# Optimization experiments

Measured on AMD Instinct MI355X. Metric: run time of the kernel, lower is better.

The kernel has to match this reference:

```python
import jax, jax.numpy as jnp
import numpy as np

NUM_HEADS = 8
HIDDEN_DIM = 64
N_REAL = 30000
N_VIRT = 2000
N_NODES = N_REAL + N_VIRT
N_EDGES = 512000
VOCAB = 100000


def setup_inputs() -> dict:
    key = jax.random.key(0)
    k1, k2, k3, k4, k5 = jax.random.split(key, 5)
    features = jax.random.normal(k1, (VOCAB, HIDDEN_DIM), dtype=jnp.float32)
    virtue_emb = jax.random.normal(k2, (N_VIRT, HIDDEN_DIM), dtype=jnp.float32)  # nn.Embedding weight ~ N(0,1)
    cnodes = jax.random.randint(k3, (N_REAL,), 0, VOCAB, dtype=jnp.int64)
    src = jax.random.randint(k4, (N_EDGES,), 0, N_NODES, dtype=jnp.int64)
    dst = jax.random.randint(k5, (N_EDGES,), 0, N_NODES, dtype=jnp.int64)
    vm_idx = jnp.arange(N_VIRT, dtype=jnp.int64) + N_REAL  # virtual nodes are appended after real nodes
    return {"features": features, "virtue_emb": virtue_emb, "cnodes": cnodes,
            "src": src, "dst": dst, "vm_idx": vm_idx}


def _edge_softmax(e, dst, n_nodes):
    # DGL edge_softmax: softmax over incoming edges of each destination node.
    m = jax.ops.segment_max(e, dst, num_segments=n_nodes)          # [N,H,1]
    ex = jnp.exp(e - m[dst])                                       # [E,H,1]
    s = jax.ops.segment_sum(ex, dst, num_segments=n_nodes)        # [N,H,1]
    return ex / s[dst]


def reference(features, virtue_emb, cnodes, src, dst, vm_idx):
    real_ndata = features[cnodes]                                  # [R,D] F.embedding
    ndata = jnp.concatenate([real_ndata, virtue_emb], axis=0)      # [N,D]
    n = ndata.shape[0]
    # agg_type='neighbor': cat([h]*H, dim=1).view(-1,H,D) == broadcast along head dim
    nft = jnp.broadcast_to(ndata[:, None, :], (n, NUM_HEADS, HIDDEN_DIM))
    e = jnp.ones((src.shape[0], NUM_HEADS, 1), dtype=ndata.dtype)
    eft = _edge_softmax(e, dst, n)                                 # [E,H,1]
    new_nft = jax.ops.segment_sum(nft[src] * eft, dst, num_segments=n)      # round 1: u_mul_e / sum
    final_nft = jax.ops.segment_sum(new_nft[src] * eft, dst, num_segments=n)  # round 2
    return final_nft[vm_idx]                                       # [V,H,D]
```

## Files before the change

### kernel.cpp

```cpp
#include <hip/hip_runtime.h>

constexpr int HEADS  = 8;
constexpr int DIM    = 64;
constexpr int NREAL  = 30000;
constexpr int NVIRT  = 2000;
constexpr int NNODES = NREAL + NVIRT;
constexpr int NEDGES = 512000;
constexpr int STRIDE = 64;

typedef _Float16 half4 __attribute__((ext_vector_type(4)));


__global__ __launch_bounds__(256) void k_prep(const float* __restrict__ features,
                                              const float* __restrict__ virtue,
                                              const int* __restrict__ cnodes,
                                              const int* __restrict__ src,
                                              const int* __restrict__ dst,
                                              _Float16* __restrict__ ndata,
                                              int* __restrict__ cnt,
                                              unsigned char* __restrict__ mark,
                                              unsigned short* __restrict__ slots) {
  int i = blockIdx.x * blockDim.x + threadIdx.x;
  {
    int node = i >> 4;
    int q    = i & 15;
    const float4* srcp = (node < NREAL)
        ? (const float4*)(features + (long)cnodes[node] * DIM)
        : (const float4*)(virtue + (long)(node - NREAL) * DIM);
    float4 v = srcp[q];
    half4 h = { (_Float16)v.x, (_Float16)v.y, (_Float16)v.z, (_Float16)v.w };
    ((half4*)(ndata + (long)node * DIM))[q] = h;
  }
  {
    int d = dst[i];
    int s = src[i];
    int pos = atomicAdd(&cnt[d], 1);
    if (pos < STRIDE) slots[(long)d * STRIDE + pos] = (unsigned short)s;
    if (d >= NREAL) mark[s] = 1;
  }
}

__global__ __launch_bounds__(256) void k_agg1(const int* __restrict__ cnt,
                                              const unsigned char* __restrict__ mark,
                                              const unsigned short* __restrict__ slots,
                                              const _Float16* __restrict__ ndata,
                                              float* __restrict__ new_nft) {
  int node = blockIdx.x * 4 + (threadIdx.x >> 6);
  if (node >= NNODES) return;
  int lane = threadIdx.x & 63;
  int q = lane >> 4;
  int l = lane & 15;
  unsigned char m = mark[node];
  int deg = cnt[node];
  int myidx = (int)slots[(long)node * STRIDE + lane];
  if (!m) return;
  if (deg > STRIDE) deg = STRIDE;
  float4 acc  = make_float4(0.f, 0.f, 0.f, 0.f);
  float4 acc2 = make_float4(0.f, 0.f, 0.f, 0.f);
  const half4* nd = (const half4*)ndata;
#pragma unroll
  for (int u = 0; u < 8; ++u) {
    int ka = u * 8 + q;
    int kb = u * 8 + q + 4;
    int sa = __shfl(myidx, ka);
    int sb = __shfl(myidx, kb);
    if (ka < deg) {
      half4 v = nd[(long)sa * 16 + l];
      acc.x += (float)v.x; acc.y += (float)v.y; acc.z += (float)v.z; acc.w += (float)v.w;
    }
    if (kb < deg) {
      half4 v = nd[(long)sb * 16 + l];
      acc2.x += (float)v.x; acc2.y += (float)v.y; acc2.z += (float)v.z; acc2.w += (float)v.w;
    }
  }
  acc.x += acc2.x; acc.y += acc2.y; acc.z += acc2.z; acc.w += acc2.w;
  acc.x += __shfl_xor(acc.x, 16); acc.y += __shfl_xor(acc.y, 16);
  acc.z += __shfl_xor(acc.z, 16); acc.w += __shfl_xor(acc.w, 16);
  acc.x += __shfl_xor(acc.x, 32); acc.y += __shfl_xor(acc.y, 32);
  acc.z += __shfl_xor(acc.z, 32); acc.w += __shfl_xor(acc.w, 32);
  if (q == 0) {
    float inv = (deg > 0) ? 1.0f / (float)deg : 0.0f;
    acc.x *= inv; acc.y *= inv; acc.z *= inv; acc.w *= inv;
    ((float4*)new_nft)[(long)node * 16 + l] = acc;
  }
}

__global__ __launch_bounds__(256) void k_agg2(const int* __restrict__ cnt,
                                              const unsigned short* __restrict__ slots,
                                              const float* __restrict__ new_nft,
                                              float* __restrict__ out) {
  int v = blockIdx.x * 4 + (threadIdx.x >> 6);
  if (v >= NVIRT) return;
  int node = NREAL + v;
  int lane = threadIdx.x & 63;
  int q = lane >> 4;
  int l = lane & 15;
  int deg = cnt[node];
  int myidx = (int)slots[(long)node * STRIDE + lane];
  if (deg > STRIDE) deg = STRIDE;
  float4 acc  = make_float4(0.f, 0.f, 0.f, 0.f);
  float4 acc2 = make_float4(0.f, 0.f, 0.f, 0.f);
  const float4* nf4 = (const float4*)new_nft;
#pragma unroll
  for (int u = 0; u < 8; ++u) {
    int ka = u * 8 + q;
    int kb = u * 8 + q + 4;
    int sa = __shfl(myidx, ka);
    int sb = __shfl(myidx, kb);
    if (ka < deg) {
      float4 x = nf4[(long)sa * 16 + l];
      acc.x += x.x; acc.y += x.y; acc.z += x.z; acc.w += x.w;
    }
    if (kb < deg) {
      float4 x = nf4[(long)sb * 16 + l];
      acc2.x += x.x; acc2.y += x.y; acc2.z += x.z; acc2.w += x.w;
    }
  }
  acc.x += acc2.x; acc.y += acc2.y; acc.z += acc2.z; acc.w += acc2.w;
  acc.x += __shfl_xor(acc.x, 16); acc.y += __shfl_xor(acc.y, 16);
  acc.z += __shfl_xor(acc.z, 16); acc.w += __shfl_xor(acc.w, 16);
  acc.x += __shfl_xor(acc.x, 32); acc.y += __shfl_xor(acc.y, 32);
  acc.z += __shfl_xor(acc.z, 32); acc.w += __shfl_xor(acc.w, 32);
  if (q == 0) {
    float inv = (deg > 0) ? 1.0f / (float)deg : 0.0f;
    acc.x *= inv; acc.y *= inv; acc.z *= inv; acc.w *= inv;
    float4* o4 = (float4*)out;
#pragma unroll
    for (int h = 0; h < HEADS; ++h)
      o4[((long)v * HEADS + h) * 16 + l] = acc;
  }
}


extern "C" void kernel_launch(void* const* d_in, const int* in_sizes, int n_in,
                              void* d_out, int out_size, void* d_ws, size_t ws_size,
                              hipStream_t stream) {
  const float* features = (const float*)d_in[0];
  const float* virtue   = (const float*)d_in[1];
  const int*   cnodes   = (const int*)d_in[2];
  const int*   src      = (const int*)d_in[3];
  const int*   dst      = (const int*)d_in[4];
  float* out = (float*)d_out;

  float*          new_nft = (float*)d_ws;
  _Float16*       ndata   = (_Float16*)(new_nft + (long)NNODES * DIM);
  int*            cnt     = (int*)(ndata + (long)NNODES * DIM);
  unsigned char*  mark    = (unsigned char*)(cnt + NNODES);
  unsigned short* slots   = (unsigned short*)(mark + NNODES);

  const int B = 256;

  hipMemsetAsync(cnt, 0, NNODES * sizeof(int) + NNODES, stream);
  k_prep<<<NEDGES / B, B, 0, stream>>>(features, virtue, cnodes, src, dst,
                                       ndata, cnt, mark, slots);
  k_agg1<<<(NNODES + 3) / 4, B, 0, stream>>>(cnt, mark, slots, ndata, new_nft);
  k_agg2<<<(NVIRT + 3) / 4, B, 0, stream>>>(cnt, slots, new_nft, out);
}
```

Baseline: 128.4 us.

## Bucket edge adjacency building into shared-memory per-block node ranges

Replaces the global-atomic adjacency build with 256 bucket blocks. Each block scans the whole destination list, compacted to 16-bit by a new pre-pass kernel, and keeps counts and slots for its 125-node range in shared memory before writing them out with coalesced stores. This removes contended global atomics and scattered slot writes, and also drops the memset. In exchange, every bucket block reads all 512K destinations (about 1 MB each, so 256 MB of mostly-L2 traffic), and slot order within a node now depends on scheduling.

```diff
diff --git a/kernel.cpp b/kernel.cpp
--- a/kernel.cpp
+++ b/kernel.cpp
@@ -8,20 +8,40 @@
 constexpr int NEDGES = 512000;
 constexpr int STRIDE = 64;
 
+constexpr int NSTAGE   = 2000;
+constexpr int NBUCKET  = 256;
+constexpr int NPB      = NNODES / NBUCKET;
+
 typedef _Float16 half4 __attribute__((ext_vector_type(4)));
 
+
+__global__ __launch_bounds__(256) void k_pre(const int* __restrict__ dst,
+                                             unsigned short* __restrict__ dst16,
+                                             unsigned int* __restrict__ mark32) {
+  int t = blockIdx.x * 256 + threadIdx.x;
+  if (t < NEDGES / 4) {
+    int4 v = ((const int4*)dst)[t];
+    ushort4 w = make_ushort4((unsigned short)v.x, (unsigned short)v.y,
+                             (unsigned short)v.z, (unsigned short)v.w);
+    ((ushort4*)dst16)[t] = w;
+  }
+  if (t < NNODES / 4) mark32[t] = 0;
+}
 
 __global__ __launch_bounds__(256) void k_prep(const float* __restrict__ features,
                                               const float* __restrict__ virtue,
                                               const int* __restrict__ cnodes,
                                               const int* __restrict__ src,
-                                              const int* __restrict__ dst,
+                                              const unsigned short* __restrict__ dst16,
                                               _Float16* __restrict__ ndata,
                                               int* __restrict__ cnt,
                                               unsigned char* __restrict__ mark,
                                               unsigned short* __restrict__ slots) {
-  int i = blockIdx.x * blockDim.x + threadIdx.x;
-  {
+  __shared__ int            cntloc[NPB];
+  __shared__ unsigned short slotbuf[NPB * STRIDE];
+
+  if (blockIdx.x < NSTAGE) {
+    int i = blockIdx.x * 256 + threadIdx.x;
     int node = i >> 4;
     int q    = i & 15;
     const float4* srcp = (node < NREAL)
@@ -30,14 +50,40 @@
     float4 v = srcp[q];
     half4 h = { (_Float16)v.x, (_Float16)v.y, (_Float16)v.z, (_Float16)v.w };
     ((half4*)(ndata + (long)node * DIM))[q] = h;
-  }
-  {
-    int d = dst[i];
-    int s = src[i];
-    int pos = atomicAdd(&cnt[d], 1);
-    if (pos < STRIDE) slots[(long)d * STRIDE + pos] = (unsigned short)s;
-    if (d >= NREAL) mark[s] = 1;
-  }
+    return;
+  }
+
+  int b    = blockIdx.x - NSTAGE;
+  int base = b * NPB;
+  bool isVirtOwner = (base >= NREAL);
+
+  if (threadIdx.x < NPB) cntloc[threadIdx.x] = 0;
+  __syncthreads();
+
+  const ushort4* d4 = (const ushort4*)dst16;
+  constexpr int ITERS = NEDGES / (256 * 4);
+  for (int it = 0; it < ITERS; ++it) {
+    int v4 = it * 256 + threadIdx.x;
+    ushort4 dv = d4[v4];
+    int e0 = v4 * 4;
+#pragma unroll
+    for (int j = 0; j < 4; ++j) {
+      int d = (j == 0) ? dv.x : (j == 1) ? dv.y : (j == 2) ? dv.z : dv.w;
+      unsigned r = (unsigned)(d - base);
+      if (r < (unsigned)NPB) {
+        int s = src[e0 + j];
+        int pos = atomicAdd(&cntloc[r], 1);
+        if (pos < STRIDE) slotbuf[r * STRIDE + pos] = (unsigned short)s;
+        if (isVirtOwner) mark[s] = 1;
+      }
+    }
+  }
+  __syncthreads();
+
+  unsigned int* gslots = (unsigned int*)(slots + (long)base * STRIDE);
+  const unsigned int* lsl = (const unsigned int*)slotbuf;
+  for (int k = threadIdx.x; k < NPB * STRIDE / 2; k += 256) gslots[k] = lsl[k];
+  if (threadIdx.x < NPB) cnt[base + threadIdx.x] = cntloc[threadIdx.x];
 }
 
 __global__ __launch_bounds__(256) void k_agg1(const int* __restrict__ cnt,
@@ -147,12 +193,13 @@
   int*            cnt     = (int*)(ndata + (long)NNODES * DIM);
   unsigned char*  mark    = (unsigned char*)(cnt + NNODES);
   unsigned short* slots   = (unsigned short*)(mark + NNODES);
+  unsigned short* dst16   = (unsigned short*)new_nft;
 
   const int B = 256;
 
-  hipMemsetAsync(cnt, 0, NNODES * sizeof(int) + NNODES, stream);
-  k_prep<<<NEDGES / B, B, 0, stream>>>(features, virtue, cnodes, src, dst,
-                                       ndata, cnt, mark, slots);
+  k_pre<<<500, B, 0, stream>>>(dst, dst16, (unsigned int*)mark);
+  k_prep<<<NSTAGE + NBUCKET, B, 0, stream>>>(features, virtue, cnodes, src,
+                                             dst16, ndata, cnt, mark, slots);
   k_agg1<<<(NNODES + 3) / 4, B, 0, stream>>>(cnt, mark, slots, ndata, new_nft);
   k_agg2<<<(NVIRT + 3) / 4, B, 0, stream>>>(cnt, slots, new_nft, out);
 }
```

Result: slower. 349.6 us (+172.1%).

## Replace global atomic slot scatter with two-pass shared-memory binning

Applied to the files above, without the earlier changes.

Edge-to-destination bucketing no longer uses per-edge global atomics on a count array. Instead, edges are first partitioned into 256 destination bins of 125 nodes using shared-memory histograms and a fixed-capacity staging buffer. A second kernel then prefix-sums each bin's per-block counts and builds the per-node slot lists in shared memory before writing them out with coalesced stores. The host memset is removed, and the mark array is now cleared inside the prep kernel. The cost is an extra launch, a binary search per edge, and a dependence on fixed capacities (48 per bin/block pair, 15-bit source packing) that hold for these input sizes.

```diff
diff --git a/kernel.cpp b/kernel.cpp
--- a/kernel.cpp
+++ b/kernel.cpp
@@ -8,6 +8,12 @@
 constexpr int NEDGES = 512000;
 constexpr int STRIDE = 64;
 
+constexpr int NSTAGE  = 2000;
+constexpr int NBINBLK = 250;
+constexpr int NBIN    = 256;
+constexpr int NPB     = 125;
+constexpr int CAP     = 48;
+
 typedef _Float16 half4 __attribute__((ext_vector_type(4)));
 
 
@@ -17,11 +23,11 @@
                                               const int* __restrict__ src,
                                               const int* __restrict__ dst,
                                               _Float16* __restrict__ ndata,
-                                              int* __restrict__ cnt,
-                                              unsigned char* __restrict__ mark,
-                                              unsigned short* __restrict__ slots) {
-  int i = blockIdx.x * blockDim.x + threadIdx.x;
-  {
+                                              unsigned short* __restrict__ gHist,
+                                              unsigned int* __restrict__ part,
+                                              unsigned int* __restrict__ mark32) {
+  if (blockIdx.x < NSTAGE) {
+    int i = blockIdx.x * 256 + threadIdx.x;
     int node = i >> 4;
     int q    = i & 15;
     const float4* srcp = (node < NREAL)
@@ -30,14 +36,94 @@
     float4 v = srcp[q];
     half4 h = { (_Float16)v.x, (_Float16)v.y, (_Float16)v.z, (_Float16)v.w };
     ((half4*)(ndata + (long)node * DIM))[q] = h;
-  }
-  {
-    int d = dst[i];
-    int s = src[i];
-    int pos = atomicAdd(&cnt[d], 1);
-    if (pos < STRIDE) slots[(long)d * STRIDE + pos] = (unsigned short)s;
+    return;
+  }
+
+  __shared__ unsigned int hist[NBIN];
+  __shared__ unsigned int cur[NBIN];
+  int b   = blockIdx.x - NSTAGE;
+  int tid = threadIdx.x;
+
+  if (b < 32) {
+    int t32 = b * 256 + tid;
+    if (t32 < NNODES / 4) mark32[t32] = 0;
+  }
+
+  hist[tid] = 0;
+  __syncthreads();
+
+  int e0 = b * 2048 + tid * 8;
+  int4 sa = *(const int4*)(src + e0);
+  int4 sb = *(const int4*)(src + e0 + 4);
+  int4 da = *(const int4*)(dst + e0);
+  int4 db = *(const int4*)(dst + e0 + 4);
+  int ds8[8] = { da.x, da.y, da.z, da.w, db.x, db.y, db.z, db.w };
+  int ss8[8] = { sa.x, sa.y, sa.z, sa.w, sb.x, sb.y, sb.z, sb.w };
+  int bn8[8];
+#pragma unroll
+  for (int j = 0; j < 8; ++j) {
+    bn8[j] = ds8[j] / NPB;
+    atomicAdd(&hist[bn8[j]], 1u);
+  }
+  __syncthreads();
+
+  gHist[tid * 256 + b] = (unsigned short)hist[tid];
+  cur[tid] = ((unsigned)tid * 256u + (unsigned)b) * CAP;
+  __syncthreads();
+
+#pragma unroll
+  for (int j = 0; j < 8; ++j) {
+    unsigned p   = atomicAdd(&cur[bn8[j]], 1u);
+    unsigned lim = ((unsigned)bn8[j] * 256u + (unsigned)b) * CAP + CAP;
+    if (p < lim)
+      part[p] = ((unsigned)ds8[j] << 15) | (unsigned)ss8[j];
+  }
+}
+
+__global__ __launch_bounds__(256) void k_bin2(const unsigned short* __restrict__ gHist,
+                                              const unsigned int* __restrict__ part,
+                                              int* __restrict__ cnt,
+                                              unsigned char* __restrict__ mark,
+                                              unsigned short* __restrict__ slots) {
+  __shared__ unsigned short slotbuf[NPB * STRIDE];
+  __shared__ int            cntloc[NPB];
+  __shared__ unsigned int   pre[257];
+
+  int B = blockIdx.x, tid = threadIdx.x;
+  if (tid < NPB) cntloc[tid] = 0;
+
+  unsigned c = (tid < NBINBLK) ? (unsigned)gHist[B * 256 + tid] : 0u;
+  if (c > CAP) c = CAP;
+  pre[tid + 1] = c;
+  if (tid == 0) pre[0] = 0;
+  __syncthreads();
+  for (int off = 1; off < 256; off <<= 1) {
+    unsigned v = 0;
+    if (tid >= off) v = pre[tid + 1 - off];
+    __syncthreads();
+    pre[tid + 1] += v;
+    __syncthreads();
+  }
+  unsigned T = pre[256];
+  int base0 = B * NPB;
+
+  for (unsigned t = tid; t < T; t += 256) {
+    int lo = 0, hi = 255;
+    while (lo < hi) { int mid = (lo + hi + 1) >> 1; if (pre[mid] <= t) lo = mid; else hi = mid - 1; }
+    unsigned w = part[((unsigned)B * 256u + (unsigned)lo) * CAP + (t - pre[lo])];
+    int d = (int)(w >> 15);
+    int s = (int)(w & 0x7fffu);
+    int r = d - base0;
+    int pos = atomicAdd(&cntloc[r], 1);
+    if (pos < STRIDE) slotbuf[r * STRIDE + pos] = (unsigned short)s;
     if (d >= NREAL) mark[s] = 1;
   }
+  __syncthreads();
+
+  unsigned int* gs = (unsigned int*)(slots + (long)base0 * STRIDE);
+  const unsigned int* ls = (const unsigned int*)slotbuf;
+  for (int k = tid; k < NPB * STRIDE / 2; k += 256) gs[k] = ls[k];
+  if (tid < NPB) cnt[base0 + tid] = cntloc[tid];
 }
 
 __global__ __launch_bounds__(256) void k_agg1(const int* __restrict__ cnt,
@@ -147,12 +233,14 @@
   int*            cnt     = (int*)(ndata + (long)NNODES * DIM);
   unsigned char*  mark    = (unsigned char*)(cnt + NNODES);
   unsigned short* slots   = (unsigned short*)(mark + NNODES);
+  unsigned short* gHist   = slots + (long)NNODES * STRIDE;
+  unsigned int*   part    = (unsigned int*)(gHist + NBIN * 256);
 
   const int B = 256;
 
-  hipMemsetAsync(cnt, 0, NNODES * sizeof(int) + NNODES, stream);
-  k_prep<<<NEDGES / B, B, 0, stream>>>(features, virtue, cnodes, src, dst,
-                                       ndata, cnt, mark, slots);
+  k_prep<<<NSTAGE + NBINBLK, B, 0, stream>>>(features, virtue, cnodes, src, dst,
+                                             ndata, gHist, part, (unsigned int*)mark);
+  k_bin2<<<NBIN, B, 0, stream>>>(gHist, part, cnt, mark, slots);
   k_agg1<<<(NNODES + 3) / 4, B, 0, stream>>>(cnt, mark, slots, ndata, new_nft);
   k_agg2<<<(NVIRT + 3) / 4, B, 0, stream>>>(cnt, slots, new_nft, out);
 }
```

Result: faster. 121.6 us (-5.4%).
